# Kernel optimization log

Hardware: AMD Instinct MI355X
Metric: run time of the kernel (lower is better)

## Reference

```python
import jax, jax.numpy as jnp
import numpy as np

MIN_RES = np.array([16, 16, 16, 16], dtype=np.float64)
MAX_RES = np.array([256, 256, 256, 128], dtype=np.float64)
NUM_SCALES = 16
MAX_PARAMS = 2 ** 19
FEATS = 2
B = 131072
PRIMES = np.array([1, 2654435761, 805459861, 3674653429], dtype=np.uint64)


def _level_meta():
    # replicates HashEncoderHyFluid.__init__ table layout
    b = np.exp((np.log(MAX_RES) - np.log(MIN_RES)) / (NUM_SCALES - 1))
    shapes, sizes, ind, offs = [], [], [], []
    total = 0
    for s in range(NUM_SCALES):
        res = np.ceil(MIN_RES * np.power(b, s)).astype(int)
        raw = np.int64(res[0] + 1) * np.int64(res[1] + 1) * np.int64(res[2] + 1) * np.int64(res[3] + 1)
        p = int(raw) if raw % 8 == 0 else int((raw + 8 - 1) / 8) * 8
        p = min(MAX_PARAMS, p)
        shapes.append(res)
        sizes.append(p)
        ind.append(1 if raw <= p else 0)
        offs.append(total)
        total += p * FEATS
    return (np.array(shapes, np.int32), np.array(sizes, np.uint32),
            np.array(ind, np.int32), np.array(offs, np.int32), total)


def setup_inputs() -> dict:
    key = jax.random.key(0)
    k1, k2 = jax.random.split(key)
    shapes, sizes, ind, offs, total = _level_meta()
    xyzts = jax.random.uniform(k1, (B, 4), dtype=jnp.float32)
    table = (jax.random.uniform(k2, (total,), dtype=jnp.float32) * 2.0 - 1.0) * 1e-4
    return {
        'xyzts': xyzts,
        'table': table,
        'shapes': jnp.asarray(shapes, jnp.int32),
        'sizes': jnp.asarray(sizes, jnp.uint32),
        'indicator': jnp.asarray(ind, jnp.int32),
        'offsets': jnp.asarray(offs, jnp.int32),
    }


def _encode(xyzts, table, shapes, sizes, indicator, offsets):
    n, L = xyzts.shape[0], shapes.shape[0]
    resf = shapes.astype(jnp.float32)                      # [L,4]
    pos = xyzts[:, None, :] * resf[None]                   # [B,L,4]
    grid_f = jnp.clip(jnp.floor(pos), 0.0, resf[None] - 1.0)
    frac = jnp.clip(pos - grid_f, 0.0, 1.0)                # [B,L,4]
    grid = grid_f.astype(jnp.uint32)                       # [B,L,4]
    # under_hash strides: prod_{i<d}(res[i]+1), uint32 wrap like taichi
    res1 = (shapes + 1).astype(jnp.uint32)                 # [L,4]
    strides = jnp.concatenate(
        [jnp.ones((L, 1), jnp.uint32), jnp.cumprod(res1[:, :3], axis=1)], axis=1)  # [L,4]
    bits = ((jnp.arange(16)[:, None] >> jnp.arange(4)[None, :]) & 1)  # [16,4]
    bits_u = bits.astype(jnp.uint32)
    w = jnp.ones((1, 1, 16), dtype=pos.dtype)
    fast = jnp.zeros((n, L, 16), jnp.uint32)
    under = jnp.zeros((n, L, 16), jnp.uint32)
    for d in range(4):  # static unroll over the 4 coordinate dims
        c = grid[:, :, None, d] + bits_u[None, None, :, d]          # [B,L,16]
        t = frac[:, :, None, d]                                     # [B,L,1]
        w = w * jnp.where(bits[None, None, :, d] == 1, t, 1.0 - t)  # [B,L,16]
        fast = fast ^ (c * jnp.uint32(int(PRIMES[d])))
        under = under + c * strides[None, :, None, d]
    h = jnp.where(indicator[None, :, None] == 1, under, fast) % sizes[None, :, None]
    it = offsets[None, :, None] + h.astype(jnp.int32) * 2           # [B,L,16]
    f0 = table[it]
    f1 = table[it + 1]
    out0 = jnp.sum(w * f0, axis=-1)                                 # [B,L]
    out1 = jnp.sum(w * f1, axis=-1)                                 # [B,L]
    return jnp.stack([out0, out1], axis=-1).reshape(n, L * 2)


def reference(xyzts, table, shapes, sizes, indicator, offsets):
    return _encode(xyzts, table, shapes, sizes, indicator, offsets)
```

## Files before the change

### kernel.cpp

```cpp
#include <hip/hip_runtime.h>

#define PRIME1 2654435761u
#define PRIME2 805459861u
#define PRIME3 3674653429u

__global__ __launch_bounds__(256) void hash_enc_kernel(
    const float* __restrict__ xyzts,
    const float* __restrict__ table,
    const int* __restrict__ shapes,
    const unsigned int* __restrict__ sizes,
    const int* __restrict__ indicator,
    const int* __restrict__ offsets,
    float* __restrict__ out,
    int npts, int nchunks)
{
    int b = blockIdx.x;
    int half = b / (nchunks * 8);
    int within = b % (nchunks * 8);
    int level = (within & 7) + (half << 3);
    int chunk = within >> 3;
    int n = chunk * 256 + (int)threadIdx.x;
    if (n >= npts) return;

    int4 rs = reinterpret_cast<const int4*>(shapes)[level];
    unsigned int size = sizes[level];
    unsigned int msk = size - 1u;
    bool ind = (indicator[level] != 0);
    int off = offsets[level];

    float4 x = reinterpret_cast<const float4*>(xyzts)[n];

    float r0 = (float)rs.x, r1 = (float)rs.y, r2 = (float)rs.z, r3 = (float)rs.w;
    float p0 = x.x * r0, p1 = x.y * r1, p2 = x.z * r2, p3 = x.w * r3;
    float g0 = fminf(fmaxf(floorf(p0), 0.f), r0 - 1.f);
    float g1 = fminf(fmaxf(floorf(p1), 0.f), r1 - 1.f);
    float g2 = fminf(fmaxf(floorf(p2), 0.f), r2 - 1.f);
    float g3 = fminf(fmaxf(floorf(p3), 0.f), r3 - 1.f);
    float f0 = fminf(fmaxf(p0 - g0, 0.f), 1.f);
    float f1 = fminf(fmaxf(p1 - g1, 0.f), 1.f);
    float f2 = fminf(fmaxf(p2 - g2, 0.f), 1.f);
    float f3 = fminf(fmaxf(p3 - g3, 0.f), 1.f);
    unsigned int u0 = (unsigned int)g0, u1 = (unsigned int)g1;
    unsigned int u2 = (unsigned int)g2, u3 = (unsigned int)g3;

    unsigned int s1 = (unsigned int)(rs.x + 1);
    unsigned int s2 = s1 * (unsigned int)(rs.y + 1);
    unsigned int s3 = s2 * (unsigned int)(rs.z + 1);

    unsigned int a1 = u1 * PRIME1, a2 = u2 * PRIME2, a3 = u3 * PRIME3;
    unsigned int xb = u0 ^ a1 ^ a2 ^ a3;
    unsigned int e0 = u0 ^ (u0 + 1u);
    unsigned int e1 = a1 ^ ((u1 + 1u) * PRIME1);
    unsigned int e2 = a2 ^ ((u2 + 1u) * PRIME2);
    unsigned int e3 = a3 ^ ((u3 + 1u) * PRIME3);

    unsigned int ab = u0 + u1 * s1 + u2 * s2 + u3 * s3;

    float om0 = 1.f - f0, om1 = 1.f - f1, om2 = 1.f - f2, om3 = 1.f - f3;

    const float* tb = table + off;

    float acc0 = 0.f, acc1 = 0.f;
#pragma unroll
    for (int c = 0; c < 16; ++c) {
        unsigned int hf = xb, hu = ab;
        if (c & 1) { hf ^= e0; hu += 1u; }
        if (c & 2) { hf ^= e1; hu += s1; }
        if (c & 4) { hf ^= e2; hu += s2; }
        if (c & 8) { hf ^= e3; hu += s3; }
        unsigned int h = ind ? hu : (hf & msk);
        float2 tv = *reinterpret_cast<const float2*>(tb + 2u * h);
        float w = (c & 1) ? f0 : om0;
        w *= (c & 2) ? f1 : om1;
        w *= (c & 4) ? f2 : om2;
        w *= (c & 8) ? f3 : om3;
        acc0 += w * tv.x;
        acc1 += w * tv.y;
    }

    reinterpret_cast<float2*>(out)[n * 16 + level] = make_float2(acc0, acc1);
}

extern "C" void kernel_launch(void* const* d_in, const int* in_sizes, int n_in,
                              void* d_out, int out_size, void* d_ws, size_t ws_size,
                              hipStream_t stream) {
    const float* xyzts = (const float*)d_in[0];
    const float* table = (const float*)d_in[1];
    const int* shapes = (const int*)d_in[2];
    const unsigned int* sizes = (const unsigned int*)d_in[3];
    const int* indicator = (const int*)d_in[4];
    const int* offsets = (const int*)d_in[5];
    float* out = (float*)d_out;

    int npts = in_sizes[0] / 4;
    int nchunks = (npts + 255) / 256;
    int blocks = nchunks * 16;
    hash_enc_kernel<<<blocks, 256, 0, stream>>>(xyzts, table, shapes, sizes,
                                                indicator, offsets, out,
                                                npts, nchunks);
}
```

Baseline: 132.7 us.

## Write level-major workspace with nontemporal stores, then transpose to output

```diff
diff --git a/kernel.cpp b/kernel.cpp
--- a/kernel.cpp
+++ b/kernel.cpp
@@ -4,6 +4,10 @@
 #define PRIME2 805459861u
 #define PRIME3 3674653429u
 
+typedef float f2v __attribute__((ext_vector_type(2)));
+typedef float f4v __attribute__((ext_vector_type(4)));
+
+template <bool DIRECT>
 __global__ __launch_bounds__(256) void hash_enc_kernel(
     const float* __restrict__ xyzts,
     const float* __restrict__ table,
@@ -11,7 +15,7 @@
     const unsigned int* __restrict__ sizes,
     const int* __restrict__ indicator,
     const int* __restrict__ offsets,
-    float* __restrict__ out,
+    float* __restrict__ dst,
     int npts, int nchunks)
 {
     int b = blockIdx.x;
@@ -78,7 +82,34 @@
         acc1 += w * tv.y;
     }
 
-    reinterpret_cast<float2*>(out)[n * 16 + level] = make_float2(acc0, acc1);
+    f2v res;
+    res.x = acc0; res.y = acc1;
+    if (DIRECT) {
+        reinterpret_cast<f2v*>(dst)[(size_t)n * 16 + level] = res;
+    } else {
+        __builtin_nontemporal_store(
+            res, reinterpret_cast<f2v*>(dst) + (size_t)level * npts + n);
+    }
+}
+
+__global__ __launch_bounds__(256) void transpose_kernel(
+    const float* __restrict__ ws, float* __restrict__ out, int npts)
+{
+    int n = blockIdx.x * 256 + (int)threadIdx.x;
+    if (n >= npts) return;
+    const f2v* w = reinterpret_cast<const f2v*>(ws);
+    f2v v[16];
+#pragma unroll
+    for (int l = 0; l < 16; ++l)
+        v[l] = w[(size_t)l * npts + n];
+    f4v* o = reinterpret_cast<f4v*>(out + (size_t)n * 32);
+#pragma unroll
+    for (int j = 0; j < 8; ++j) {
+        f4v q;
+        q.x = v[2 * j].x; q.y = v[2 * j].y;
+        q.z = v[2 * j + 1].x; q.w = v[2 * j + 1].y;
+        __builtin_nontemporal_store(q, o + j);
+    }
 }
 
 extern "C" void kernel_launch(void* const* d_in, const int* in_sizes, int n_in,
@@ -95,7 +126,15 @@
     int npts = in_sizes[0] / 4;
     int nchunks = (npts + 255) / 256;
     int blocks = nchunks * 16;
-    hash_enc_kernel<<<blocks, 256, 0, stream>>>(xyzts, table, shapes, sizes,
-                                                indicator, offsets, out,
-                                                npts, nchunks);
+
+    size_t ws_needed = (size_t)npts * 16 * 2 * sizeof(float);
+    if (ws_size >= ws_needed) {
+        float* ws = (float*)d_ws;
+        hash_enc_kernel<false><<<blocks, 256, 0, stream>>>(
+            xyzts, table, shapes, sizes, indicator, offsets, ws, npts, nchunks);
+        transpose_kernel<<<nchunks, 256, 0, stream>>>(ws, out, npts);
+    } else {
+        hash_enc_kernel<true><<<blocks, 256, 0, stream>>>(
+            xyzts, table, shapes, sizes, indicator, offsets, out, npts, nchunks);
+    }
 }
```

New measurement: 134.9 us. About the same (+1.7%).
